# Optimization experiments

Hardware: AMD Instinct MI355X
Metric: run time of the kernel (lower is better)

Reference implementation:

```python
import jax, jax.numpy as jnp
import numpy as np

B, S, D = 4, 4096, 1024
DECAY = 0.95


def setup_inputs() -> dict:
    key = jax.random.key(0)
    ks = jax.random.split(key, 7)
    sc = 1.0 / np.sqrt(D)
    return {
        "h": jax.random.normal(ks[0], (B, S, D), jnp.float32),
        "chunk_size": 128,
        "Wq": jax.random.normal(ks[1], (D, D), jnp.float32) * sc,
        "Wk": jax.random.normal(ks[2], (D, D), jnp.float32) * sc,
        "Wv": jax.random.normal(ks[3], (D, D), jnp.float32) * sc,
        "Wo": jax.random.normal(ks[4], (D, D), jnp.float32) * sc,
        "Wg": jax.random.normal(ks[5], (D, D), jnp.float32) * sc,
        "bg": jnp.zeros((D,), jnp.float32),
    }


def reference(h, chunk_size, Wq, Wk, Wv, Wo, Wg, bg):
    bsz, seq_len, d_model = h.shape
    n_chunks = seq_len // chunk_size  # S divisible by chunk_size

    # projections (torch nn.Linear: y = x @ W.T)
    q = jnp.einsum('bsd,ed->bse', h, Wq)
    k = jnp.einsum('bsd,ed->bse', h, Wk)
    v = jnp.einsum('bsd,ed->bse', h, Wv)
    gate = jax.nn.sigmoid(jnp.einsum('bsd,ed->bse', h, Wg) + bg)

    def to_chunks(x):  # [B,S,D] -> [n_chunks, B, T, D]
        return x.reshape(bsz, n_chunks, chunk_size, d_model).transpose(1, 0, 2, 3)

    qc, kc, vc, gc = map(to_chunks, (q, k, v, gate))

    def step(state, inp):
        q_c, k_c, v_c, g_c = inp
        kv = jnp.einsum('btd,bte->bde', k_c, v_c) / chunk_size
        state = DECAY * state + (1.0 - DECAY) * kv
        ret = jnp.einsum('btd,bde->bte', q_c, state)
        return state, ret * g_c

    state0 = jnp.zeros((bsz, d_model, d_model), h.dtype)
    _, out_chunks = jax.lax.scan(step, state0, (qc, kc, vc, gc))
    out = out_chunks.transpose(1, 0, 2, 3).reshape(bsz, seq_len, d_model)
    return jnp.einsum('bsd,ed->bse', out, Wo)
```

## Files before the change

kernel.cpp:

```cpp
#include <hip/hip_runtime.h>
#include <math.h>

#define B_ 4
#define S_ 4096
#define D_ 1024
#define T_ 128
#define NC_ 32
#define DECAY_ 0.95f
#define NPAIR_ 528

typedef __bf16 bf16;
typedef __bf16 bf16x8 __attribute__((ext_vector_type(8)));
typedef __bf16 bf16x4 __attribute__((ext_vector_type(4)));
typedef float f32x4 __attribute__((ext_vector_type(4)));

__device__ __forceinline__ f32x4 mfma16(bf16x8 a, bf16x8 b, f32x4 c) {
  return __builtin_amdgcn_mfma_f32_16x16x32_bf16(a, b, c, 0, 0, 0);
}

__device__ __forceinline__ void gload16(const bf16* g, bf16* l) {
  __builtin_amdgcn_global_load_lds(
      (const __attribute__((address_space(1))) unsigned int*)g,
      (__attribute__((address_space(3))) unsigned int*)l, 16, 0, 0);
}

__global__ void cast_kernel(const float* __restrict__ src, bf16* __restrict__ dst, int n) {
  int i = (blockIdx.x * blockDim.x + threadIdx.x) * 4;
  int stride = gridDim.x * blockDim.x * 4;
  for (; i < n; i += stride) {
    float4 f = *(const float4*)(src + i);
    bf16x4 o = { (bf16)f.x, (bf16)f.y, (bf16)f.z, (bf16)f.w };
    *(bf16x4*)(dst + i) = o;
  }
}

__global__ void wcast_kernel(const float* __restrict__ Wq, const float* __restrict__ Wk,
                             const float* __restrict__ Wv, const float* __restrict__ Wg,
                             const float* __restrict__ Wo,
                             bf16* __restrict__ Wcat, bf16* __restrict__ Wo_bf) {
  const int NW = 1 << 20;
  long gid = ((long)blockIdx.x * blockDim.x + threadIdx.x) * 4;
  int sel = (int)(gid >> 20);
  int off = (int)(gid & (NW - 1));
  const float* src = (sel == 0) ? Wq : (sel == 1) ? Wk : (sel == 2) ? Wv
                   : (sel == 3) ? Wg : Wo;
  bf16* dst = (sel < 4) ? (Wcat + (long)sel * NW) : Wo_bf;
  float4 f = *(const float4*)(src + off);
  bf16x4 o = { (bf16)f.x, (bf16)f.y, (bf16)f.z, (bf16)f.w };
  *(bf16x4*)(dst + off) = o;
}

__global__ __launch_bounds__(512, 1) void gemm_proj(
    const bf16* __restrict__ A, const bf16* __restrict__ W,
    const float* __restrict__ bg,
    bf16* __restrict__ qo, bf16* __restrict__ ko,
    bf16* __restrict__ vT, bf16* __restrict__ go)
{
  __shared__ __align__(16) bf16 As[2][256 * 64];
  __shared__ __align__(16) bf16 Bs[2][256 * 64];
  const int K = 1024;
  const int NT = 16;
  int m0 = blockIdx.y * 256;
  int n0 = blockIdx.x * 256;
  int t = threadIdx.x;
  int l = t & 63, w = t >> 6;
  int wr = w >> 2, wc = w & 3;

  const bf16* Ab = A + (long)m0 * K;
  const bf16* Wb = W + (long)n0 * K;

  int srow_off = t >> 3;
  int scol_swz = (((t & 7) ^ ((t >> 3) & 7)) * 8);
  int wdst = w << 9;

  f32x4 acc[8][4] = {};

  auto stage = [&](int buf, int kt) {
#pragma unroll
    for (int c = 0; c < 4; ++c) {
      int r = c * 64 + srow_off;
      gload16(Ab + (long)r * K + kt * 64 + scol_swz, &As[buf][c * 4096 + wdst]);
      gload16(Wb + (long)r * K + kt * 64 + scol_swz, &Bs[buf][c * 4096 + wdst]);
    }
  };

  auto compute = [&](int buf) {
    bf16x8 bfrag[4][2];
#pragma unroll
    for (int fn = 0; fn < 4; ++fn)
#pragma unroll
      for (int ks = 0; ks < 2; ++ks) {
        int rb = wc * 64 + fn * 16 + (l & 15);
        int sb = ks * 4 + (l >> 4);
        bfrag[fn][ks] = *(const bf16x8*)(&Bs[buf][rb * 64 + ((sb ^ (rb & 7)) * 8)]);
      }
#pragma unroll
    for (int fm = 0; fm < 8; ++fm) {
      int ra = wr * 128 + fm * 16 + (l & 15);
      int s0 = (l >> 4);
      bf16x8 a0 = *(const bf16x8*)(&As[buf][ra * 64 + ((s0 ^ (ra & 7)) * 8)]);
      bf16x8 a1 = *(const bf16x8*)(&As[buf][ra * 64 + (((s0 + 4) ^ (ra & 7)) * 8)]);
#pragma unroll
      for (int fn = 0; fn < 4; ++fn) {
        acc[fm][fn] = mfma16(a0, bfrag[fn][0], acc[fm][fn]);
        acc[fm][fn] = mfma16(a1, bfrag[fn][1], acc[fm][fn]);
      }
    }
  };

  stage(0, 0);
  stage(1, 1);
  for (int kt = 0; kt < NT; ++kt) {
    if (kt < NT - 1) {
      asm volatile("s_waitcnt vmcnt(8)" ::: "memory");
    } else {
      asm volatile("s_waitcnt vmcnt(0)" ::: "memory");
    }
    __builtin_amdgcn_s_barrier();
    __builtin_amdgcn_sched_barrier(0);
    compute(kt & 1);
    __builtin_amdgcn_s_barrier();
    if (kt + 2 < NT) stage(kt & 1, kt + 2);
  }

  int widx = n0 >> 10;
  int b = m0 >> 12;

#pragma unroll
  for (int fm = 0; fm < 8; ++fm) {
    int rowg = m0 + wr * 128 + fm * 16 + (l >> 4) * 4;
#pragma unroll
    for (int fn = 0; fn < 4; ++fn) {
      int col = (n0 & 1023) + wc * 64 + fn * 16 + (l & 15);
      if (widx == 2) {
        int chunk = (rowg & 4095) >> 7;
        int trow = rowg & 127;
        bf16x4 pk = { (bf16)acc[fm][fn][0], (bf16)acc[fm][fn][1],
                      (bf16)acc[fm][fn][2], (bf16)acc[fm][fn][3] };
        *(bf16x4*)(vT + ((long)(b * NC_ + chunk) * D_ + col) * T_ + trow) = pk;
      } else if (widx < 2) {
        bf16* dst = (widx == 0) ? qo : ko;
#pragma unroll
        for (int r = 0; r < 4; ++r)
          dst[(long)(rowg + r) * D_ + col] = (bf16)acc[fm][fn][r];
      } else {
        float bgv = bg[col];
#pragma unroll
        for (int r = 0; r < 4; ++r) {
          float x = acc[fm][fn][r] + bgv;
          go[(long)(rowg + r) * D_ + col] = (bf16)(1.0f / (1.0f + __expf(-x)));
        }
      }
    }
  }
}

__global__ __launch_bounds__(256) void qk_kernel(
    const bf16* __restrict__ q, const bf16* __restrict__ k,
    bf16* __restrict__ Plo, bf16* __restrict__ Phi)
{
  __shared__ __align__(16) bf16 As[128 * 32];
  __shared__ __align__(16) bf16 Bs[128 * 32];
  const int K = 1024;
  int p = blockIdx.x, b = blockIdx.y;
  int n = (int)((sqrtf(8.f * (float)p + 1.f) - 1.f) * 0.5f);
  while ((n + 1) * (n + 2) / 2 <= p) ++n;
  while (n * (n + 1) / 2 > p) --n;
  int j = p - n * (n + 1) / 2;

  int tid = threadIdx.x;
  int l = tid & 63, w = tid >> 6;
  int wr = w >> 1, wc = w & 1;
  int wbase = w << 9;

  const bf16* Ab = q + (long)(b * S_ + n * T_) * K;
  const bf16* Wb = k + (long)(b * S_ + j * T_) * K;
  int lrow = tid >> 2, lcol = (tid & 3) * 8;

  f32x4 acc[4][4] = {};

  for (int k0 = 0; k0 < K; k0 += 32) {
    gload16(Ab + (long)lrow * K + k0 + lcol, As + wbase);
    gload16(Ab + (long)(lrow + 64) * K + k0 + lcol, As + 2048 + wbase);
    gload16(Wb + (long)lrow * K + k0 + lcol, Bs + wbase);
    gload16(Wb + (long)(lrow + 64) * K + k0 + lcol, Bs + 2048 + wbase);
    __syncthreads();
    bf16x8 af[4], bfr[4];
#pragma unroll
    for (int m = 0; m < 4; ++m)
      af[m] = *(const bf16x8*)(As + (wr * 64 + m * 16 + (l & 15)) * 32 + (l >> 4) * 8);
#pragma unroll
    for (int nn = 0; nn < 4; ++nn)
      bfr[nn] = *(const bf16x8*)(Bs + (wc * 64 + nn * 16 + (l & 15)) * 32 + (l >> 4) * 8);
#pragma unroll
    for (int m = 0; m < 4; ++m)
#pragma unroll
      for (int nn = 0; nn < 4; ++nn)
        acc[m][nn] = mfma16(af[m], bfr[nn], acc[m][nn]);
    __syncthreads();
  }

  float c = powf(DECAY_, (float)(n - j)) * ((1.0f - DECAY_) / (float)T_);
  int tile = b * NPAIR_ + p;
  bf16* Pt = (tile < 1024) ? (Plo + (long)tile * 16384)
                           : (Phi + (long)(tile - 1024) * 16384);

#pragma unroll
  for (int m = 0; m < 4; ++m) {
    int row = wr * 64 + m * 16 + (l >> 4) * 4;
#pragma unroll
    for (int nn = 0; nn < 4; ++nn) {
      int col = wc * 64 + nn * 16 + (l & 15);
#pragma unroll
      for (int r = 0; r < 4; ++r)
        Pt[(long)(row + r) * T_ + col] = (bf16)(acc[m][nn][r] * c);
    }
  }
}

__global__ __launch_bounds__(256) void pv_kernel(
    const bf16* __restrict__ Plo, const bf16* __restrict__ Phi,
    const bf16* __restrict__ vT, const bf16* __restrict__ g,
    bf16* __restrict__ mid)
{
  __shared__ __align__(16) bf16 As[128 * 32];
  __shared__ __align__(16) bf16 Bs[128 * 32];
  int et = blockIdx.x;
  int n  = 31 - blockIdx.y;
  int b  = blockIdx.z;
  int e0 = et * 128;
  int tid = threadIdx.x, l = tid & 63, w = tid >> 6;
  int wr = w >> 1, wc = w & 1;
  int wbase = w << 9;
  int lrow = tid >> 2, lcol = (tid & 3) * 8;
  int pbase = b * NPAIR_ + n * (n + 1) / 2;

  f32x4 acc[4][4] = {};

  for (int j = 0; j <= n; ++j) {
    int tile = pbase + j;
    const bf16* Pt = (tile < 1024) ? (Plo + (long)tile * 16384)
                                   : (Phi + (long)(tile - 1024) * 16384);
    const bf16* Vt = vT + (long)(b * NC_ + j) * D_ * T_ + (long)e0 * T_;
#pragma unroll
    for (int kk = 0; kk < 4; ++kk) {
      int k0 = kk * 32;
      gload16(Pt + (long)lrow * T_ + k0 + lcol, As + wbase);
      gload16(Pt + (long)(lrow + 64) * T_ + k0 + lcol, As + 2048 + wbase);
      gload16(Vt + (long)lrow * T_ + k0 + lcol, Bs + wbase);
      gload16(Vt + (long)(lrow + 64) * T_ + k0 + lcol, Bs + 2048 + wbase);
      __syncthreads();
      bf16x8 af[4], bv[4];
#pragma unroll
      for (int m = 0; m < 4; ++m)
        af[m] = *(const bf16x8*)(As + (wr * 64 + m * 16 + (l & 15)) * 32 + (l >> 4) * 8);
#pragma unroll
      for (int nn = 0; nn < 4; ++nn)
        bv[nn] = *(const bf16x8*)(Bs + (wc * 64 + nn * 16 + (l & 15)) * 32 + (l >> 4) * 8);
#pragma unroll
      for (int m = 0; m < 4; ++m)
#pragma unroll
        for (int nn = 0; nn < 4; ++nn)
          acc[m][nn] = mfma16(af[m], bv[nn], acc[m][nn]);
      __syncthreads();
    }
  }

#pragma unroll
  for (int m = 0; m < 4; ++m) {
    int trow = n * T_ + wr * 64 + m * 16 + (l >> 4) * 4;
#pragma unroll
    for (int nn = 0; nn < 4; ++nn) {
      int col = e0 + wc * 64 + nn * 16 + (l & 15);
#pragma unroll
      for (int r = 0; r < 4; ++r) {
        long idx = ((long)b * S_ + trow + r) * D_ + col;
        float gv = (float)g[idx];
        mid[idx] = (bf16)(acc[m][nn][r] * gv);
      }
    }
  }
}

__global__ __launch_bounds__(256) void gemm_out(
    const bf16* __restrict__ A, const bf16* __restrict__ W,
    float* __restrict__ C)
{
  __shared__ __align__(16) bf16 As[128 * 32];
  __shared__ __align__(16) bf16 Bs[128 * 32];
  const int K = 1024;
  int m0 = blockIdx.y * 128;
  int n0 = blockIdx.x * 128;
  int tid = threadIdx.x;
  int l = tid & 63, w = tid >> 6;
  int wr = w >> 1, wc = w & 1;
  int wbase = w << 9;

  const bf16* Ab = A + (long)m0 * K;
  const bf16* Wb = W + (long)n0 * K;
  int lrow = tid >> 2, lcol = (tid & 3) * 8;

  f32x4 acc[4][4] = {};

  for (int k0 = 0; k0 < K; k0 += 32) {
    gload16(Ab + (long)lrow * K + k0 + lcol, As + wbase);
    gload16(Ab + (long)(lrow + 64) * K + k0 + lcol, As + 2048 + wbase);
    gload16(Wb + (long)lrow * K + k0 + lcol, Bs + wbase);
    gload16(Wb + (long)(lrow + 64) * K + k0 + lcol, Bs + 2048 + wbase);
    __syncthreads();
    bf16x8 af[4], bfr[4];
#pragma unroll
    for (int m = 0; m < 4; ++m)
      af[m] = *(const bf16x8*)(As + (wr * 64 + m * 16 + (l & 15)) * 32 + (l >> 4) * 8);
#pragma unroll
    for (int n = 0; n < 4; ++n)
      bfr[n] = *(const bf16x8*)(Bs + (wc * 64 + n * 16 + (l & 15)) * 32 + (l >> 4) * 8);
#pragma unroll
    for (int m = 0; m < 4; ++m)
#pragma unroll
      for (int n = 0; n < 4; ++n)
        acc[m][n] = mfma16(af[m], bfr[n], acc[m][n]);
    __syncthreads();
  }

#pragma unroll
  for (int m = 0; m < 4; ++m) {
    int row = m0 + wr * 64 + m * 16 + (l >> 4) * 4;
#pragma unroll
    for (int n = 0; n < 4; ++n) {
      int col = n0 + wc * 64 + n * 16 + (l & 15);
#pragma unroll
      for (int r = 0; r < 4; ++r)
        C[(long)(row + r) * D_ + col] = acc[m][n][r];
    }
  }
}

extern "C" void kernel_launch(void* const* d_in, const int* in_sizes, int n_in,
                              void* d_out, int out_size, void* d_ws, size_t ws_size,
                              hipStream_t stream) {
  const float* h  = (const float*)d_in[0];
  const float* Wq = (const float*)d_in[2];
  const float* Wk = (const float*)d_in[3];
  const float* Wv = (const float*)d_in[4];
  const float* Wo = (const float*)d_in[5];
  const float* Wg = (const float*)d_in[6];
  const float* bg = (const float*)d_in[7];
  float* out = (float*)d_out;

  bf16* ws = (bf16*)d_ws;
  const long NHD = (long)B_ * S_ * D_;
  const long NW  = (long)D_ * D_;

  bf16* h_bf  = ws;  ws += NHD;
  bf16* Wcat  = ws;  ws += 4 * NW;
  bf16* Wo_bf = ws;  ws += NW;
  bf16* q_bf  = ws;  ws += NHD;
  bf16* k_bf  = ws;  ws += NHD;
  bf16* vT    = ws;  ws += NHD;
  bf16* g_bf  = ws;  ws += NHD;
  bf16* P_hi  = ws;  ws += (long)(4 * NPAIR_ - 1024) * 16384;

  bf16* P_lo = h_bf;
  bf16* mid  = q_bf;

  cast_kernel<<<4096, 256, 0, stream>>>(h, h_bf, (int)NHD);
  wcast_kernel<<<5120, 256, 0, stream>>>(Wq, Wk, Wv, Wg, Wo, Wcat, Wo_bf);

  gemm_proj<<<dim3(16, 64), 512, 0, stream>>>(h_bf, Wcat, bg, q_bf, k_bf, vT, g_bf);
  qk_kernel<<<dim3(NPAIR_, 4), 256, 0, stream>>>(q_bf, k_bf, P_lo, P_hi);
  pv_kernel<<<dim3(8, 32, 4), 256, 0, stream>>>(P_lo, P_hi, vT, g_bf, mid);
  gemm_out<<<dim3(8, 128), 256, 0, stream>>>(mid, Wo_bf, out);
}
```

Baseline: 599.2 us.

## Double-buffer and enlarge tiles in qk, pv and output GEMM kernels

Rewrites the three post-projection kernels to use 512-thread blocks with larger tiles (256-wide outputs, K-step 64), XOR-swizzled LDS layouts and a two-stage double-buffered global_load_lds pipeline gated by explicit vmcnt waits. The qk kernel now computes two causal chunk pairs per block, sharing the q tile. The goal is to raise data reuse, hide load latency behind MFMA work and cut LDS bank conflicts. In exchange, larger LDS footprints limit occupancy to one block per CU, grids shrink, and the odd-n duplicate pair wastes some compute.

```diff
diff --git a/kernel.cpp b/kernel.cpp
--- a/kernel.cpp
+++ b/kernel.cpp
@@ -155,183 +155,288 @@
   }
 }
 
-__global__ __launch_bounds__(256) void qk_kernel(
+__global__ __launch_bounds__(512, 1) void qk_kernel(
     const bf16* __restrict__ q, const bf16* __restrict__ k,
     bf16* __restrict__ Plo, bf16* __restrict__ Phi)
 {
-  __shared__ __align__(16) bf16 As[128 * 32];
-  __shared__ __align__(16) bf16 Bs[128 * 32];
+  __shared__ __align__(16) bf16 As[2][128 * 64];
+  __shared__ __align__(16) bf16 Bs[2][256 * 64];
   const int K = 1024;
-  int p = blockIdx.x, b = blockIdx.y;
-  int n = (int)((sqrtf(8.f * (float)p + 1.f) - 1.f) * 0.5f);
-  while ((n + 1) * (n + 2) / 2 <= p) ++n;
-  while (n * (n + 1) / 2 > p) --n;
-  int j = p - n * (n + 1) / 2;
-
-  int tid = threadIdx.x;
-  int l = tid & 63, w = tid >> 6;
-  int wr = w >> 1, wc = w & 1;
-  int wbase = w << 9;
+  const int NT = 16;
+  int pb = blockIdx.x, b = blockIdx.y;
+  int n = 0, base = 0;
+  while (base + ((n + 2) >> 1) <= pb) { base += (n + 2) >> 1; ++n; }
+  int jj = pb - base;
+  int j0 = jj * 2;
+  int j1v = j0 + 1;
+  int j1 = (j1v <= n) ? j1v : j0;
+
+  int t = threadIdx.x;
+  int l = t & 63, w = t >> 6;
+  int wr = (w >> 2) & 1, wc = w & 3;
 
   const bf16* Ab = q + (long)(b * S_ + n * T_) * K;
-  const bf16* Wb = k + (long)(b * S_ + j * T_) * K;
-  int lrow = tid >> 2, lcol = (tid & 3) * 8;
+  const bf16* K0 = k + (long)(b * S_ + j0 * T_) * K;
+  const bf16* K1 = k + (long)(b * S_ + j1 * T_) * K;
+
+  int srow_off = t >> 3;
+  int scol_swz = (((t & 7) ^ ((t >> 3) & 7)) * 8);
+  int wdst = w << 9;
 
   f32x4 acc[4][4] = {};
 
-  for (int k0 = 0; k0 < K; k0 += 32) {
-    gload16(Ab + (long)lrow * K + k0 + lcol, As + wbase);
-    gload16(Ab + (long)(lrow + 64) * K + k0 + lcol, As + 2048 + wbase);
-    gload16(Wb + (long)lrow * K + k0 + lcol, Bs + wbase);
-    gload16(Wb + (long)(lrow + 64) * K + k0 + lcol, Bs + 2048 + wbase);
-    __syncthreads();
-    bf16x8 af[4], bfr[4];
-#pragma unroll
-    for (int m = 0; m < 4; ++m)
-      af[m] = *(const bf16x8*)(As + (wr * 64 + m * 16 + (l & 15)) * 32 + (l >> 4) * 8);
-#pragma unroll
-    for (int nn = 0; nn < 4; ++nn)
-      bfr[nn] = *(const bf16x8*)(Bs + (wc * 64 + nn * 16 + (l & 15)) * 32 + (l >> 4) * 8);
-#pragma unroll
-    for (int m = 0; m < 4; ++m)
-#pragma unroll
-      for (int nn = 0; nn < 4; ++nn)
-        acc[m][nn] = mfma16(af[m], bfr[nn], acc[m][nn]);
-    __syncthreads();
-  }
-
-  float c = powf(DECAY_, (float)(n - j)) * ((1.0f - DECAY_) / (float)T_);
-  int tile = b * NPAIR_ + p;
-  bf16* Pt = (tile < 1024) ? (Plo + (long)tile * 16384)
-                           : (Phi + (long)(tile - 1024) * 16384);
-
-#pragma unroll
-  for (int m = 0; m < 4; ++m) {
-    int row = wr * 64 + m * 16 + (l >> 4) * 4;
-#pragma unroll
-    for (int nn = 0; nn < 4; ++nn) {
-      int col = wc * 64 + nn * 16 + (l & 15);
-#pragma unroll
-      for (int r = 0; r < 4; ++r)
-        Pt[(long)(row + r) * T_ + col] = (bf16)(acc[m][nn][r] * c);
-    }
-  }
-}
-
-__global__ __launch_bounds__(256) void pv_kernel(
+  auto stage = [&](int buf, int kt) {
+#pragma unroll
+    for (int c = 0; c < 2; ++c) {
+      int r = c * 64 + srow_off;
+      gload16(Ab + (long)r * K + kt * 64 + scol_swz, &As[buf][c * 4096 + wdst]);
+    }
+#pragma unroll
+    for (int c = 0; c < 4; ++c) {
+      int r = (c & 1) * 64 + srow_off;
+      const bf16* Ksrc = (c < 2) ? K0 : K1;
+      gload16(Ksrc + (long)r * K + kt * 64 + scol_swz, &Bs[buf][c * 4096 + wdst]);
+    }
+  };
+
+  auto compute = [&](int buf) {
+    bf16x8 bfrag[4][2];
+#pragma unroll
+    for (int fn = 0; fn < 4; ++fn)
+#pragma unroll
+      for (int ks = 0; ks < 2; ++ks) {
+        int rb = wc * 64 + fn * 16 + (l & 15);
+        int sb = ks * 4 + (l >> 4);
+        bfrag[fn][ks] = *(const bf16x8*)(&Bs[buf][rb * 64 + ((sb ^ (rb & 7)) * 8)]);
+      }
+#pragma unroll
+    for (int fm = 0; fm < 4; ++fm) {
+      int ra = wr * 64 + fm * 16 + (l & 15);
+      int s0 = (l >> 4);
+      bf16x8 a0 = *(const bf16x8*)(&As[buf][ra * 64 + ((s0 ^ (ra & 7)) * 8)]);
+      bf16x8 a1 = *(const bf16x8*)(&As[buf][ra * 64 + (((s0 + 4) ^ (ra & 7)) * 8)]);
+#pragma unroll
+      for (int fn = 0; fn < 4; ++fn) {
+        acc[fm][fn] = mfma16(a0, bfrag[fn][0], acc[fm][fn]);
+        acc[fm][fn] = mfma16(a1, bfrag[fn][1], acc[fm][fn]);
+      }
+    }
+  };
+
+  stage(0, 0);
+  stage(1, 1);
+  for (int kt = 0; kt < NT; ++kt) {
+    if (kt < NT - 1) {
+      asm volatile("s_waitcnt vmcnt(6)" ::: "memory");
+    } else {
+      asm volatile("s_waitcnt vmcnt(0)" ::: "memory");
+    }
+    __builtin_amdgcn_s_barrier();
+    __builtin_amdgcn_sched_barrier(0);
+    compute(kt & 1);
+    __builtin_amdgcn_s_barrier();
+    if (kt + 2 < NT) stage(kt & 1, kt + 2);
+  }
+
+  const float upd = (1.0f - DECAY_) / (float)T_;
+  int jsel = (wc < 2) ? j0 : j1v;
+  bool valid = (wc < 2) || (j1v <= n);
+  if (valid) {
+    float c = powf(DECAY_, (float)(n - jsel)) * upd;
+    int tile = b * NPAIR_ + n * (n + 1) / 2 + jsel;
+    bf16* Pt = (tile < 1024) ? (Plo + (long)tile * 16384)
+                             : (Phi + (long)(tile - 1024) * 16384);
+#pragma unroll
+    for (int fm = 0; fm < 4; ++fm) {
+      int row = wr * 64 + fm * 16 + (l >> 4) * 4;
+#pragma unroll
+      for (int fn = 0; fn < 4; ++fn) {
+        int colp = ((wc & 1) * 64) + fn * 16 + (l & 15);
+#pragma unroll
+        for (int r = 0; r < 4; ++r)
+          Pt[(long)(row + r) * T_ + colp] = (bf16)(acc[fm][fn][r] * c);
+      }
+    }
+  }
+}
+
+__global__ __launch_bounds__(512, 1) void pv_kernel(
     const bf16* __restrict__ Plo, const bf16* __restrict__ Phi,
     const bf16* __restrict__ vT, const bf16* __restrict__ g,
     bf16* __restrict__ mid)
 {
-  __shared__ __align__(16) bf16 As[128 * 32];
-  __shared__ __align__(16) bf16 Bs[128 * 32];
+  __shared__ __align__(16) bf16 As[2][128 * 64];
+  __shared__ __align__(16) bf16 Bs[2][256 * 64];
   int et = blockIdx.x;
   int n  = 31 - blockIdx.y;
   int b  = blockIdx.z;
-  int e0 = et * 128;
-  int tid = threadIdx.x, l = tid & 63, w = tid >> 6;
-  int wr = w >> 1, wc = w & 1;
-  int wbase = w << 9;
-  int lrow = tid >> 2, lcol = (tid & 3) * 8;
+  int e0 = et * 256;
+  int t = threadIdx.x;
+  int l = t & 63, w = t >> 6;
+  int wr = (w >> 2) & 1, wc = w & 3;
+
+  int srow_off = t >> 3;
+  int scol_swz = (((t & 7) ^ ((t >> 3) & 7)) * 8);
+  int wdst = w << 9;
   int pbase = b * NPAIR_ + n * (n + 1) / 2;
+  const bf16* Vbase = vT + (long)(b * NC_) * D_ * T_ + (long)e0 * T_;
 
   f32x4 acc[4][4] = {};
 
-  for (int j = 0; j <= n; ++j) {
+  auto stage = [&](int buf, int s) {
+    int j = s >> 1, kt2 = s & 1;
     int tile = pbase + j;
     const bf16* Pt = (tile < 1024) ? (Plo + (long)tile * 16384)
                                    : (Phi + (long)(tile - 1024) * 16384);
-    const bf16* Vt = vT + (long)(b * NC_ + j) * D_ * T_ + (long)e0 * T_;
-#pragma unroll
-    for (int kk = 0; kk < 4; ++kk) {
-      int k0 = kk * 32;
-      gload16(Pt + (long)lrow * T_ + k0 + lcol, As + wbase);
-      gload16(Pt + (long)(lrow + 64) * T_ + k0 + lcol, As + 2048 + wbase);
-      gload16(Vt + (long)lrow * T_ + k0 + lcol, Bs + wbase);
-      gload16(Vt + (long)(lrow + 64) * T_ + k0 + lcol, Bs + 2048 + wbase);
-      __syncthreads();
-      bf16x8 af[4], bv[4];
-#pragma unroll
-      for (int m = 0; m < 4; ++m)
-        af[m] = *(const bf16x8*)(As + (wr * 64 + m * 16 + (l & 15)) * 32 + (l >> 4) * 8);
-#pragma unroll
-      for (int nn = 0; nn < 4; ++nn)
-        bv[nn] = *(const bf16x8*)(Bs + (wc * 64 + nn * 16 + (l & 15)) * 32 + (l >> 4) * 8);
-#pragma unroll
-      for (int m = 0; m < 4; ++m)
-#pragma unroll
-        for (int nn = 0; nn < 4; ++nn)
-          acc[m][nn] = mfma16(af[m], bv[nn], acc[m][nn]);
-      __syncthreads();
-    }
-  }
-
-#pragma unroll
-  for (int m = 0; m < 4; ++m) {
-    int trow = n * T_ + wr * 64 + m * 16 + (l >> 4) * 4;
-#pragma unroll
-    for (int nn = 0; nn < 4; ++nn) {
-      int col = e0 + wc * 64 + nn * 16 + (l & 15);
+    const bf16* Vt = Vbase + (long)j * D_ * T_;
+#pragma unroll
+    for (int c = 0; c < 2; ++c) {
+      int r = c * 64 + srow_off;
+      gload16(Pt + (long)r * T_ + kt2 * 64 + scol_swz, &As[buf][c * 4096 + wdst]);
+    }
+#pragma unroll
+    for (int c = 0; c < 4; ++c) {
+      int r = c * 64 + srow_off;
+      gload16(Vt + (long)r * T_ + kt2 * 64 + scol_swz, &Bs[buf][c * 4096 + wdst]);
+    }
+  };
+
+  auto compute = [&](int buf) {
+    bf16x8 bfrag[4][2];
+#pragma unroll
+    for (int fn = 0; fn < 4; ++fn)
+#pragma unroll
+      for (int ks = 0; ks < 2; ++ks) {
+        int rb = wc * 64 + fn * 16 + (l & 15);
+        int sb = ks * 4 + (l >> 4);
+        bfrag[fn][ks] = *(const bf16x8*)(&Bs[buf][rb * 64 + ((sb ^ (rb & 7)) * 8)]);
+      }
+#pragma unroll
+    for (int fm = 0; fm < 4; ++fm) {
+      int ra = wr * 64 + fm * 16 + (l & 15);
+      int s0 = (l >> 4);
+      bf16x8 a0 = *(const bf16x8*)(&As[buf][ra * 64 + ((s0 ^ (ra & 7)) * 8)]);
+      bf16x8 a1 = *(const bf16x8*)(&As[buf][ra * 64 + (((s0 + 4) ^ (ra & 7)) * 8)]);
+#pragma unroll
+      for (int fn = 0; fn < 4; ++fn) {
+        acc[fm][fn] = mfma16(a0, bfrag[fn][0], acc[fm][fn]);
+        acc[fm][fn] = mfma16(a1, bfrag[fn][1], acc[fm][fn]);
+      }
+    }
+  };
+
+  int nsteps = 2 * (n + 1);
+  stage(0, 0);
+  stage(1, 1);
+  for (int kt = 0; kt < nsteps; ++kt) {
+    if (kt < nsteps - 1) {
+      asm volatile("s_waitcnt vmcnt(6)" ::: "memory");
+    } else {
+      asm volatile("s_waitcnt vmcnt(0)" ::: "memory");
+    }
+    __builtin_amdgcn_s_barrier();
+    __builtin_amdgcn_sched_barrier(0);
+    compute(kt & 1);
+    __builtin_amdgcn_s_barrier();
+    if (kt + 2 < nsteps) stage(kt & 1, kt + 2);
+  }
+
+#pragma unroll
+  for (int fm = 0; fm < 4; ++fm) {
+    int trow = n * T_ + wr * 64 + fm * 16 + (l >> 4) * 4;
+#pragma unroll
+    for (int fn = 0; fn < 4; ++fn) {
+      int col = e0 + wc * 64 + fn * 16 + (l & 15);
 #pragma unroll
       for (int r = 0; r < 4; ++r) {
         long idx = ((long)b * S_ + trow + r) * D_ + col;
         float gv = (float)g[idx];
-        mid[idx] = (bf16)(acc[m][nn][r] * gv);
-      }
-    }
-  }
-}
-
-__global__ __launch_bounds__(256) void gemm_out(
+        mid[idx] = (bf16)(acc[fm][fn][r] * gv);
+      }
+    }
+  }
+}
+
+__global__ __launch_bounds__(512, 1) void gemm_out(
     const bf16* __restrict__ A, const bf16* __restrict__ W,
     float* __restrict__ C)
 {
-  __shared__ __align__(16) bf16 As[128 * 32];
-  __shared__ __align__(16) bf16 Bs[128 * 32];
+  __shared__ __align__(16) bf16 As[2][256 * 64];
+  __shared__ __align__(16) bf16 Bs[2][256 * 64];
   const int K = 1024;
-  int m0 = blockIdx.y * 128;
-  int n0 = blockIdx.x * 128;
-  int tid = threadIdx.x;
-  int l = tid & 63, w = tid >> 6;
-  int wr = w >> 1, wc = w & 1;
-  int wbase = w << 9;
+  const int NT = 16;
+  int m0 = blockIdx.y * 256;
+  int n0 = blockIdx.x * 256;
+  int t = threadIdx.x;
+  int l = t & 63, w = t >> 6;
+  int wr = w >> 2, wc = w & 3;
 
   const bf16* Ab = A + (long)m0 * K;
   const bf16* Wb = W + (long)n0 * K;
-  int lrow = tid >> 2, lcol = (tid & 3) * 8;
-
-  f32x4 acc[4][4] = {};
-
-  for (int k0 = 0; k0 < K; k0 += 32) {
-    gload16(Ab + (long)lrow * K + k0 + lcol, As + wbase);
-    gload16(Ab + (long)(lrow + 64) * K + k0 + lcol, As + 2048 + wbase);
-    gload16(Wb + (long)lrow * K + k0 + lcol, Bs + wbase);
-    gload16(Wb + (long)(lrow + 64) * K + k0 + lcol, Bs + 2048 + wbase);
-    __syncthreads();
-    bf16x8 af[4], bfr[4];
-#pragma unroll
-    for (int m = 0; m < 4; ++m)
-      af[m] = *(const bf16x8*)(As + (wr * 64 + m * 16 + (l & 15)) * 32 + (l >> 4) * 8);
-#pragma unroll
-    for (int n = 0; n < 4; ++n)
-      bfr[n] = *(const bf16x8*)(Bs + (wc * 64 + n * 16 + (l & 15)) * 32 + (l >> 4) * 8);
-#pragma unroll
-    for (int m = 0; m < 4; ++m)
-#pragma unroll
-      for (int n = 0; n < 4; ++n)
-        acc[m][n] = mfma16(af[m], bfr[n], acc[m][n]);
-    __syncthreads();
-  }
-
-#pragma unroll
-  for (int m = 0; m < 4; ++m) {
-    int row = m0 + wr * 64 + m * 16 + (l >> 4) * 4;
-#pragma unroll
-    for (int n = 0; n < 4; ++n) {
-      int col = n0 + wc * 64 + n * 16 + (l & 15);
+
+  int srow_off = t >> 3;
+  int scol_swz = (((t & 7) ^ ((t >> 3) & 7)) * 8);
+  int wdst = w << 9;
+
+  f32x4 acc[8][4] = {};
+
+  auto stage = [&](int buf, int kt) {
+#pragma unroll
+    for (int c = 0; c < 4; ++c) {
+      int r = c * 64 + srow_off;
+      gload16(Ab + (long)r * K + kt * 64 + scol_swz, &As[buf][c * 4096 + wdst]);
+      gload16(Wb + (long)r * K + kt * 64 + scol_swz, &Bs[buf][c * 4096 + wdst]);
+    }
+  };
+
+  auto compute = [&](int buf) {
+    bf16x8 bfrag[4][2];
+#pragma unroll
+    for (int fn = 0; fn < 4; ++fn)
+#pragma unroll
+      for (int ks = 0; ks < 2; ++ks) {
+        int rb = wc * 64 + fn * 16 + (l & 15);
+        int sb = ks * 4 + (l >> 4);
+        bfrag[fn][ks] = *(const bf16x8*)(&Bs[buf][rb * 64 + ((sb ^ (rb & 7)) * 8)]);
+      }
+#pragma unroll
+    for (int fm = 0; fm < 8; ++fm) {
+      int ra = wr * 128 + fm * 16 + (l & 15);
+      int s0 = (l >> 4);
+      bf16x8 a0 = *(const bf16x8*)(&As[buf][ra * 64 + ((s0 ^ (ra & 7)) * 8)]);
+      bf16x8 a1 = *(const bf16x8*)(&As[buf][ra * 64 + (((s0 + 4) ^ (ra & 7)) * 8)]);
+#pragma unroll
+      for (int fn = 0; fn < 4; ++fn) {
+        acc[fm][fn] = mfma16(a0, bfrag[fn][0], acc[fm][fn]);
+        acc[fm][fn] = mfma16(a1, bfrag[fn][1], acc[fm][fn]);
+      }
+    }
+  };
+
+  stage(0, 0);
+  stage(1, 1);
+  for (int kt = 0; kt < NT; ++kt) {
+    if (kt < NT - 1) {
+      asm volatile("s_waitcnt vmcnt(8)" ::: "memory");
+    } else {
+      asm volatile("s_waitcnt vmcnt(0)" ::: "memory");
+    }
+    __builtin_amdgcn_s_barrier();
+    __builtin_amdgcn_sched_barrier(0);
+    compute(kt & 1);
+    __builtin_amdgcn_s_barrier();
+    if (kt + 2 < NT) stage(kt & 1, kt + 2);
+  }
+
+#pragma unroll
+  for (int fm = 0; fm < 8; ++fm) {
+    int rowg = m0 + wr * 128 + fm * 16 + (l >> 4) * 4;
+#pragma unroll
+    for (int fn = 0; fn < 4; ++fn) {
+      int col = n0 + wc * 64 + fn * 16 + (l & 15);
 #pragma unroll
       for (int r = 0; r < 4; ++r)
-        C[(long)(row + r) * D_ + col] = acc[m][n][r];
+        C[(long)(rowg + r) * D_ + col] = acc[fm][fn][r];
     }
   }
 }
@@ -368,7 +473,7 @@
   wcast_kernel<<<5120, 256, 0, stream>>>(Wq, Wk, Wv, Wg, Wo, Wcat, Wo_bf);
 
   gemm_proj<<<dim3(16, 64), 512, 0, stream>>>(h_bf, Wcat, bg, q_bf, k_bf, vT, g_bf);
-  qk_kernel<<<dim3(NPAIR_, 4), 256, 0, stream>>>(q_bf, k_bf, P_lo, P_hi);
-  pv_kernel<<<dim3(8, 32, 4), 256, 0, stream>>>(P_lo, P_hi, vT, g_bf, mid);
-  gemm_out<<<dim3(8, 128), 256, 0, stream>>>(mid, Wo_bf, out);
-}
+  qk_kernel<<<dim3(272, 4), 512, 0, stream>>>(q_bf, k_bf, P_lo, P_hi);
+  pv_kernel<<<dim3(4, 32, 4), 512, 0, stream>>>(P_lo, P_hi, vT, g_bf, mid);
+  gemm_out<<<dim3(4, 64), 512, 0, stream>>>(mid, Wo_bf, out);
+}
```

Measured after the change: 574.1 us. 1.04x faster.
